# Kernel tuning notes

Hardware: AMD Instinct MI355X
Metric: run time of the kernel (lower is better)

Reference implementation:

```python
import jax, jax.numpy as jnp
import numpy as np
import math

B, C, H, W_ = 64, 1024, 10, 10      # C = vis_chans = ir_chans = lan_chans = m_chans
NTOK, MTOK = H * W_, 20             # 100 image tokens (W1: 100x100), 20 text tokens (W2: 100x20)
K_NN, BIG, EPS = 8, 1.0e6, 1e-8


def _minmax(t):
    # per-sample min-max normalization over the full distance slice
    mn = t.min(axis=(1, 2), keepdims=True)
    mx = t.max(axis=(1, 2), keepdims=True)
    return (t - mn) / (mx - mn + EPS)


def _geodesic(X):
    # Isomap-style geodesic distances: symmetric 8-NN Euclidean graph + Floyd-Warshall.
    P = X.shape[0]
    sq = jnp.sum(X * X, axis=-1)
    D = jnp.sqrt(jnp.maximum(sq[:, None] + sq[None, :] - 2.0 * (X @ X.T), 0.0))
    Dm = D + jnp.eye(P, dtype=X.dtype) * BIG          # exclude self from kNN
    negd, idx = jax.lax.top_k(-Dm, K_NN)              # 8 nearest neighbors per node
    A = jnp.full((P, P), BIG, X.dtype).at[jnp.arange(P)[:, None], idx].set(-negd)
    Wg = jnp.minimum(A, A.T)                          # undirected graph
    Wg = Wg.at[jnp.diag_indices(P)].set(0.0)

    def body(Dk, k):
        return jnp.minimum(Dk, Dk[:, k][:, None] + Dk[k, :][None, :]), None

    Wg, _ = jax.lax.scan(body, Wg, jnp.arange(P))
    return Wg


def _forward(ir, vis, lan, vis_w, vis_b, vis_g, vis_be, ir_w, ir_b, ir_g, ir_be,
             t_w, t_b, vout_w, vout_b, tout_w, tout_b, W1, b1, W2, b2, W4, W5,
             ml_w, ml_b, ml2_w, ml2_b, scalars):
    lam1, lam2, a1, be1, g1, a2, be2, g2, wg_aw, wg_ab, wg_bw, wg_bb = scalars
    sqc = jnp.sqrt(jnp.float32(C))
    vis_r = vis.reshape(B, C, -1).transpose(0, 2, 1)   # [B,100,C]
    ir_r = ir.reshape(B, C, -1).transpose(0, 2, 1)     # [B,100,C]
    lan_t = lan.transpose(0, 2, 1)                     # [B,20,C]

    geo = jax.vmap(_geodesic)

    # ---- compute_M_image (detached in original) ----
    joint_vi = jnp.concatenate([vis_r, ir_r], axis=1)                    # [B,200,C]
    d_vi = jax.lax.stop_gradient(geo(joint_vi))[:, :NTOK, NTOK:]         # [B,100,100]
    M_v2i_dist = _minmax(d_vi)
    sigma = jax.lax.stop_gradient(jnp.median(M_v2i_dist))
    M_v2i_fix = jnp.exp(-M_v2i_dist ** 2 / (2.0 * sigma ** 2))
    lam1s = jax.nn.sigmoid(lam1)
    M_v2i_learn = lam1s * M_v2i_fix + (1.0 - lam1s) * (W1 * M_v2i_fix + b1)

    def conv_in_relu(x, w3, b3, g3, be3, i):
        # 1x1 conv + InstanceNorm2d(affine) + ReLU, flattened to tokens
        y = jnp.einsum('bchw,mc->bmhw', x, w3[i]) + b3[i][None, :, None, None]
        mu = y.mean((2, 3), keepdims=True)
        var = y.var((2, 3), keepdims=True)
        y = (y - mu) / jnp.sqrt(var + 1e-5) * g3[i][None, :, None, None] + be3[i][None, :, None, None]
        return jax.nn.relu(y).reshape(B, C, -1).transpose(0, 2, 1)       # [B,100,C]

    Qv, Kv, Vv = [conv_in_relu(vis, vis_w, vis_b, vis_g, vis_be, i) for i in range(3)]
    Qi, Ki, Vi = [conv_in_relu(ir, ir_w, ir_b, ir_g, ir_be, i) for i in range(3)]
    Qt, Kt, Vt = [jax.nn.relu(lan_t @ t_w[i].T + t_b[i]) for i in range(3)]

    # fusion weights from GAP of the learned manifold matrix
    Mgap = M_v2i_learn.mean((1, 2), keepdims=True)       # [B,1,1]
    alpha = jax.nn.sigmoid(wg_aw * Mgap + wg_ab)
    beta = jax.nn.sigmoid(wg_bw * Mgap + wg_bb)
    Qf, Kf, Vf = alpha * Qv + beta * Qi, alpha * Kv + beta * Ki, alpha * Vv + beta * Vi
    feat_img = alpha * vis_r + beta * ir_r               # [B,100,C]

    # ---- compute_M_text (detached in original) ----
    joint_it = jnp.concatenate([feat_img, lan_t], axis=1)                # [B,120,C]
    d_it = jax.lax.stop_gradient(geo(joint_it))
    M_i2t_dist = _minmax(d_it[:, :NTOK, NTOK:])          # [B,100,20] (unused downstream, as in original)
    M_t2i_dist = _minmax(d_it[:, NTOK:, :NTOK])          # [B,20,100]
    sigma2 = jax.lax.stop_gradient(jnp.median(M_t2i_dist))
    M_t2i_fix = jnp.exp(-M_t2i_dist ** 2 / (2.0 * sigma2 ** 2))          # [B,20,100]
    M_i2t_fix = M_t2i_fix.transpose(0, 2, 1)                             # [B,100,20]
    lam2s = jax.nn.sigmoid(lam2)
    M_i2t_lo = lam2s * M_i2t_fix + (1.0 - lam2s) * (W2 * M_i2t_fix + b2) # [B,100,20]
    M_t2i_lo = M_i2t_lo.transpose(0, 2, 1)                               # [B,20,100]
    M_t2i_lo = jax.nn.softmax(M_t2i_lo / sqc, axis=2)
    M_i2t_lo = jax.nn.softmax(M_i2t_lo / sqc, axis=2)
    M_t2i_learn = (M_i2t_lo @ lan_t) @ ml_w.T + ml_b       # [B,100,C]
    M_i2t_learn = (M_t2i_lo @ feat_img) @ ml2_w.T + ml2_b  # [B,20,C]

    # ---- text->image cross attention ----
    A = Qt @ Kf.transpose(0, 2, 1) \
        + a1 * (Qt @ M_t2i_learn.transpose(0, 2, 1)) \
        + be1 * (W4 @ (M_t2i_learn @ Kf.transpose(0, 2, 1)))
    Av = jax.nn.softmax(A / sqc, axis=2)                   # [B,20,100]
    new_lan = Av @ Vf + g1 * (M_t2i_lo @ Vf)               # [B,20,C]

    # ---- image->text cross attention ----
    Bm = Qf @ Kt.transpose(0, 2, 1) \
        + a2 * (Qf @ M_i2t_learn.transpose(0, 2, 1)) \
        + be2 * (W5 @ (M_i2t_learn @ Kt.transpose(0, 2, 1)))
    Bv = jax.nn.softmax(Bm / sqc, axis=2)                  # [B,100,20]
    new_vis = Bv @ Vt + g2 * (M_i2t_lo @ Vt)               # [B,100,C]

    new_vis = new_vis.transpose(0, 2, 1).reshape(B, C, H, W_)
    new_vis = jnp.einsum('bchw,mc->bmhw', new_vis, vout_w) + vout_b[None, :, None, None]
    new_lan = new_lan @ tout_w.T + tout_b

    # ---- regularization loss ----
    fA = jax.nn.softmax(M_t2i_fix / sqc, axis=2)
    fB = jax.nn.softmax(M_i2t_fix / sqc, axis=2)
    l1 = jnp.abs(Av - fA).mean() + jnp.abs(Bv - fB).mean()
    var = lambda x: jnp.var(x, ddof=1)                    # torch .var() is unbiased
    l2 = -jnp.abs(var(Av) - var(fA)) - jnp.abs(var(Bv) - var(fB))
    loss = (l1 + 100.0 * l2) * 1000.0
    return new_vis, new_lan, loss


def setup_inputs() -> dict:
    key = jax.random.key(0)
    ks = jax.random.split(key, 20)
    f = lambda k, s, sc=1.0: jax.random.normal(k, s, jnp.float32) * sc
    return dict(
        ir=f(ks[0], (B, C, H, W_)),
        vis=f(ks[1], (B, C, H, W_)),
        lan=f(ks[2], (B, C, MTOK)),
        vis_w=f(ks[3], (3, C, C), 0.02), vis_b=jnp.zeros((3, C), jnp.float32),
        vis_g=jnp.ones((3, C), jnp.float32), vis_be=jnp.zeros((3, C), jnp.float32),
        ir_w=f(ks[4], (3, C, C), 0.02), ir_b=jnp.zeros((3, C), jnp.float32),
        ir_g=jnp.ones((3, C), jnp.float32), ir_be=jnp.zeros((3, C), jnp.float32),
        t_w=f(ks[5], (3, C, C), 0.02), t_b=jnp.zeros((3, C), jnp.float32),
        vout_w=f(ks[6], (C, C), 0.02), vout_b=jnp.zeros((C,), jnp.float32),
        tout_w=f(ks[7], (C, C), 0.02), tout_b=jnp.zeros((C,), jnp.float32),
        W1=f(ks[8], (NTOK, NTOK), 0.1), b1=jnp.zeros((NTOK, NTOK), jnp.float32),
        W2=f(ks[9], (NTOK, MTOK), 0.1), b2=jnp.zeros((NTOK, MTOK), jnp.float32),
        W4=f(ks[10], (MTOK, NTOK), 0.1),
        W5=f(ks[11], (NTOK, MTOK), 0.1),
        ml_w=f(ks[12], (C, C), 0.02), ml_b=jnp.zeros((C,), jnp.float32),
        ml2_w=f(ks[13], (C, C), 0.02), ml2_b=jnp.zeros((C,), jnp.float32),
        # [lam1, lam2, a1, b1, g1, a2, b2, g2, wg_aw, wg_ab, wg_bw, wg_bb]
        scalars=jnp.array([0.5, 0.5, 0.5, 0.5, 0.5, 0.5, 0.5, 0.5, 0.3, 0.0, 0.3, 0.0], jnp.float32),
    )


def reference(ir, vis, lan, vis_w, vis_b, vis_g, vis_be, ir_w, ir_b, ir_g, ir_be,
              t_w, t_b, vout_w, vout_b, tout_w, tout_b, W1, b1, W2, b2, W4, W5,
              ml_w, ml_b, ml2_w, ml2_b, scalars):
    return _forward(ir, vis, lan, vis_w, vis_b, vis_g, vis_be, ir_w, ir_b, ir_g, ir_be,
                    t_w, t_b, vout_w, vout_b, tout_w, tout_b, W1, b1, W2, b2, W4, W5,
                    ml_w, ml_b, ml2_w, ml2_b, scalars)
```

## Files before the change

### kernel.cpp

```cpp
#include <hip/hip_runtime.h>
#include <hip/hip_bf16.h>
#include <math.h>

#define B_   64
#define C_   1024
#define HW   100
#define MT_  20
#define P1   200
#define P2   120
#define BIGF 1.0e6f
#define EPSF 1e-8f
#define SQC  32.0f

static constexpr size_t F_J    = 0;
static constexpr size_t N_J    = (size_t)B_*P1*C_;
static constexpr size_t F_D    = F_J + N_J;
static constexpr size_t N_D    = (size_t)B_*P1*P1;
static constexpr size_t F_SQ   = F_D + N_D;
static constexpr size_t N_SQ   = (size_t)B_*P1;
static constexpr size_t F_KNN  = F_SQ + N_SQ;
static constexpr size_t N_KNN  = (size_t)B_*P1*8;
static constexpr size_t F_MV   = F_KNN + N_KNN;
static constexpr size_t N_MV   = (size_t)B_*HW*HW;
static constexpr size_t F_MT   = F_MV + N_MV;
// ... 71 lines not shown
  int row = blockIdx.x;
  const float* r = J + (size_t)row*C_;
  float s = 0.f;
  for (int c = threadIdx.x; c < C_; c += 64){ float v = r[c]; s += v*v; }
  for (int o = 32; o > 0; o >>= 1) s += __shfl_down(s, o);
  if (threadIdx.x == 0) sq[row] = s;
}

__global__ __launch_bounds__(256) void k_gram_dist(const float* __restrict__ J,
    const float* __restrict__ sq, float* __restrict__ D, int P){
  __shared__ __align__(16) float Xi[32][68];
  __shared__ __align__(16) float Xj[32][68];
  int b = blockIdx.z;
  int r0 = blockIdx.x*64, s0 = blockIdx.y*64;
  int tx = threadIdx.x & 15, ty = threadIdx.x >> 4;
  const float* Jb = J + (size_t)b*P*C_;
  float acc[4][4];
  #pragma unroll
  for (int u = 0; u < 4; u++)
    #pragma unroll
    for (int v = 0; v < 4; v++) acc[u][v] = 0.f;
  for (int c0 = 0; c0 < C_; c0 += 32){
    for (int e = threadIdx.x; e < 2048; e += 256){
      int rr = e >> 5, cc = e & 31;
      Xi[cc][rr] = (r0+rr < P) ? Jb[(size_t)(r0+rr)*C_ + c0+cc] : 0.f;
      Xj[cc][rr] = (s0+rr < P) ? Jb[(size_t)(s0+rr)*C_ + c0+cc] : 0.f;
    }
    __syncthreads();
    for (int kk = 0; kk < 32; kk++){
      float4 xr4 = *(const float4*)&Xi[kk][ty*4];
      float4 xs4 = *(const float4*)&Xj[kk][tx*4];
      float xr[4] = {xr4.x, xr4.y, xr4.z, xr4.w};
      float xs[4] = {xs4.x, xs4.y, xs4.z, xs4.w};
      #pragma unroll
      for (int u = 0; u < 4; u++)
        #pragma unroll
        for (int v = 0; v < 4; v++) acc[u][v] += xr[u]*xs[v];
    }
    __syncthreads();
  }
  #pragma unroll
  for (int u = 0; u < 4; u++){
    #pragma unroll
    for (int v = 0; v < 4; v++){
      int r = r0 + ty*4 + u, s = s0 + tx*4 + v;
      if (r < P && s < P){
        float d2 = sq[b*P+r] + sq[b*P+s] - 2.f*acc[u][v];
        D[((size_t)b*P + r)*P + s] = sqrtf(fmaxf(d2, 0.f));
      }
    }
  }
}

template<int P>
__global__ void k_knn(const float* __restrict__ D, int* __restrict__ knn){
  constexpr int NS = (P + 63)/64;
  int row = blockIdx.x;
  int i = row % P;
  const float* Dr = D + (size_t)row*P;
  float v[NS];
  #pragma unroll
  for (int t = 0; t < NS; t++){
    int j = threadIdx.x + t*64;
    float d = (j < P) ? Dr[j] : 4.0e6f;
    if (j == i) d += BIGF;
    v[t] = d;
  }
  for (int k = 0; k < 8; k++){
    float bv = 3.4e38f; int bj = 1 << 30;
    #pragma unroll
    for (int t = 0; t < NS; t++){
      int j = threadIdx.x + t*64;
      if (v[t] < bv){ bv = v[t]; bj = j; }
    }
    for (int o = 32; o > 0; o >>= 1){
      float ov = __shfl_xor(bv, o);
      int   oj = __shfl_xor(bj, o);
      if (ov < bv || (ov == bv && oj < bj)){ bv = ov; bj = oj; }
    }
    if (threadIdx.x == 0) knn[(size_t)row*8 + k] = bj;
    if ((bj & 63) == (int)threadIdx.x){
      #pragma unroll
      for (int t = 0; t < NS; t++) if (t == (bj >> 6)) v[t] = 3.9e38f;
    }
  }
}

template<int P, int NT, int RP, int CP, int R0, int C0, int RR, int CC>
__global__ __launch_bounds__(1024) void k_fwx(const float* __restrict__ D,
    const int* __restrict__ knn, float* __restrict__ outM){
  constexpr int PR = P/RP;
  constexpr int PC = P/CP;
  constexpr int NTH = PR*PC;
  __shared__ float rowk[P], colk[P];
  __shared__ int kl[P*8];
  __shared__ float rmn[1024], rmx[1024];
  int b = blockIdx.x;
  const float* Db = D + (size_t)b*P*P;
  const int* kb = knn + (size_t)b*P*8;
  int tid = threadIdx.x;
  bool act = tid < NTH;
  int pi = tid / PC, pj = tid - pi*PC;
  int i0 = pi*RP, j0 = pj*CP;
  for (int e = tid; e < P*8; e += NT) kl[e] = kb[e];
  __syncthreads();
  float w[RP][CP];
  if (act){
    #pragma unroll
    for (int r = 0; r < RP; r++){
      float4 v = *(const float4*)(Db + (size_t)(i0+r)*P + j0);
      w[r][0]=v.x; w[r][1]=v.y; w[r][2]=v.z; w[r][3]=v.w;
      int i = i0 + r;
      #pragma unroll
      for (int c = 0; c < CP; c++){
        int j = j0 + c;
        if (i == j) w[r][c] = 0.f;
        else {
          const int* ki = &kl[i*8];
          const int* kj = &kl[j*8];
          bool e = false;
          #pragma unroll
          for (int k = 0; k < 8; k++) e = e || (ki[k] == j) || (kj[k] == i);
          if (!e) w[r][c] = BIGF;
        }
      }
    }
  }
  __syncthreads();
  for (int k = 0; k < P; k++){
    if (act){
      #pragma unroll
      for (int r = 0; r < RP; r++){
        if (i0 + r == k)
          *(float4*)(rowk + j0) = make_float4(w[r][0],w[r][1],w[r][2],w[r][3]);
      }
      #pragma unroll
      for (int c = 0; c < CP; c++){
        if (j0 + c == k){
          #pragma unroll
          for (int r = 0; r < RP; r++) colk[i0+r] = w[r][c];
        }
      }
    }
    __syncthreads();
    if (act){
      float4 rk4 = *(const float4*)(rowk + j0);
      float rk[4] = {rk4.x, rk4.y, rk4.z, rk4.w};
      float ck[RP];
      #pragma unroll
      for (int r = 0; r < RP; r++) ck[r] = colk[i0+r];
      #pragma unroll
      for (int r = 0; r < RP; r++)
        #pragma unroll
        for (int c = 0; c < CP; c++)
          w[r][c] = fminf(w[r][c], ck[r] + rk[c]);
    }
    __syncthreads();
  }
  float mn = 3.4e38f, mx = -3.4e38f;
  if (act){
    #pragma unroll
    for (int r = 0; r < RP; r++){
      int i = i0 + r;
      if (i >= R0 && i < R0+RR){
        #pragma unroll
        for (int c = 0; c < CP; c++){
          int j = j0 + c;
          if (j >= C0 && j < C0+CC){
            mn = fminf(mn, w[r][c]); mx = fmaxf(mx, w[r][c]);
          }
        }
      }
    }
  }
  rmn[tid] = mn; rmx[tid] = mx;
  __syncthreads();
  for (int o = 512; o > 0; o >>= 1){
    if (tid < o && tid + o < NT){
      rmn[tid] = fminf(rmn[tid], rmn[tid+o]);
      rmx[tid] = fmaxf(rmx[tid], rmx[tid+o]);
    }
    __syncthreads();
  }
  mn = rmn[0]; mx = rmx[0];
  float inv = 1.f/(mx - mn + EPSF);
  if (act){
    #pragma unroll
    for (int r = 0; r < RP; r++){
      int i = i0 + r;
      if (i >= R0 && i < R0+RR){
        #pragma unroll
        for (int c = 0; c < CP; c++){
          int j = j0 + c;
          if (j >= C0 && j < C0+CC)
            outM[((size_t)b*RR + (i-R0))*CC + (j-C0)] = (w[r][c] - mn)*inv;
        }
      }
    }
  }
}

__global__ void k_med_init(float* hs){ if (threadIdx.x == 0){ hs[0] = 0.f; hs[1] = 1.0f; } }

__global__ __launch_bounds__(256) void k_med_hist(const float* __restrict__ x, int N,
                           const float* __restrict__ hs, unsigned* __restrict__ hist){
  __shared__ unsigned lh[1025];
  for (int i = threadIdx.x; i < 1025; i += 256) lh[i] = 0u;
  __syncthreads();
  float lo = hs[0], hi = hs[1];
  float scale = 1024.f/(hi - lo);
  unsigned below = 0;
  int idx = blockIdx.x*256 + threadIdx.x;
  int stride = gridDim.x*256;
  for (int i = idx; i < N; i += stride){
    float v = x[i];
    if (v < lo) below++;
    else if (v < hi){
      int bn = (int)((v - lo)*scale);
      if (bn > 1023) bn = 1023;
      atomicAdd(&lh[bn], 1u);
    }
  }
  for (int o = 32; o > 0; o >>= 1) below += __shfl_down(below, o);
  if ((threadIdx.x & 63) == 0 && below) atomicAdd(&lh[1024], below);
  __syncthreads();
  for (int i = threadIdx.x; i < 1025; i += 256){
    unsigned v = lh[i];
    if (v) atomicAdd(&hist[i], v);
  }
}

__global__ void k_med_select(float* hs, const unsigned* __restrict__ hist, int k){
  if (threadIdx.x != 0) return;
  float lo = hs[0], hi = hs[1], w = (hi - lo)*(1.f/1024.f);
  unsigned cum = hist[1024];
  int bf = 1023;
  for (int bn = 0; bn < 1024; bn++){
    unsigned h = hist[bn];
    if (cum + h > (unsigned)k){ bf = bn; break; }
    cum += h;
  }
  hs[0] = lo + bf*w; hs[1] = lo + (bf+1)*w;
}

__global__ __launch_bounds__(256) void k_mgap(const float* __restrict__ Mv,
    const float* __restrict__ W1, const float* __restrict__ b1,
    const float* __restrict__ sc, const float* __restrict__ hs,
    float* __restrict__ alpha, float* __restrict__ bet){
  __shared__ float sr[256];
  int b = blockIdx.x;
  float lam1s = 1.f/(1.f + expf(-sc[0]));
  float sig = 0.5f*(hs[0] + hs[1]);
  float inv2s = 1.f/(2.f*sig*sig);
  const float* Mb = Mv + (size_t)b*HW*HW;
  float s = 0.f;
  for (int e = threadIdx.x; e < HW*HW; e += 256){
    float v = Mb[e];
    float f = expf(-v*v*inv2s);
    s += lam1s*f + (1.f - lam1s)*(W1[e]*f + b1[e]);
  }
  sr[threadIdx.x] = s; __syncthreads();
  for (int o = 128; o > 0; o >>= 1){
    if ((int)threadIdx.x < o) sr[threadIdx.x] += sr[threadIdx.x+o];
    __syncthreads();
  }
  if (threadIdx.x == 0){
    float mg = sr[0]*(1.f/(HW*HW));
    alpha[b] = 1.f/(1.f + expf(-(sc[8]*mg + sc[9])));
    bet[b]   = 1.f/(1.f + expf(-(sc[10]*mg + sc[11])));
  }
}

__global__ void k_castw(const float* __restrict__ a, const float* __restrict__ b,
                        short* __restrict__ oa, short* __restrict__ ob){
  int i = (blockIdx.x*256 + threadIdx.x)*4;
  if (i >= 3*C_*C_) return;
  float4 va = *(const float4*)(a + i);
  float4 vb = *(const float4*)(b + i);
  short ra[4] = { f2bf(va.x), f2bf(va.y), f2bf(va.z), f2bf(va.w) };
  short rb[4] = { f2bf(vb.x), f2bf(vb.y), f2bf(vb.z), f2bf(vb.w) };
  *(bhalf*)(oa + i) = *(bhalf*)ra;
  *(bhalf*)(ob + i) = *(bhalf*)rb;
}

__global__ void k_cast(const float* __restrict__ a, short* __restrict__ oa, int n){
  int i = (blockIdx.x*256 + threadIdx.x)*4;
  if (i >= n) return;
  float4 va = *(const float4*)(a + i);
  short ra[4] = { f2bf(va.x), f2bf(va.y), f2bf(va.z), f2bf(va.w) };
  *(bhalf*)(oa + i) = *(bhalf*)ra;
}

__global__ void k_cast2(const float* __restrict__ a, const float* __restrict__ b,
                        short* __restrict__ oa, short* __restrict__ ob,
                        int n1, int n2){
// ... 91 lines not shown
      bfrag axv = zf, axi = zf;
      if (tf*16 + lr < HW){
        axv = *(const bfrag*)(xvp + (size_t)tf*16*C_ + k0);
        axi = *(const bfrag*)(xip + (size_t)tf*16*C_ + k0);
      }
      acc[tf][0][0] = MFMA_B16(axv, bw0v, acc[tf][0][0]);
      acc[tf][1][0] = MFMA_B16(axv, bw1v, acc[tf][1][0]);
      acc[tf][0][1] = MFMA_B16(axi, bw0i, acc[tf][0][1]);
      acc[tf][1][1] = MFMA_B16(axi, bw1i, acc[tf][1][1]);
    }
  }
  float al = alpha[b], bt = bet[b];
  float* ob = out + ((size_t)(wsel*B_ + b))*HW*C_;
  #pragma unroll
  for (int mf = 0; mf < 2; mf++){
    int m = m0 + w*32 + mf*16 + lr;
    float s1v=0.f,s2v=0.f,s1i=0.f,s2i=0.f;
    #pragma unroll
    for (int tf = 0; tf < 7; tf++){
      #pragma unroll
      for (int r = 0; r < 4; r++){
        int t = tf*16 + lg*4 + r;
        if (t < HW){
          float yv = acc[tf][mf][0][r], yi = acc[tf][mf][1][r];
          s1v += yv; s2v += yv*yv; s1i += yi; s2i += yi*yi;
        }
      }
    }
    s1v += __shfl_xor(s1v,16); s1v += __shfl_xor(s1v,32);
    s2v += __shfl_xor(s2v,16); s2v += __shfl_xor(s2v,32);
    s1i += __shfl_xor(s1i,16); s1i += __shfl_xor(s1i,32);
    s2i += __shfl_xor(s2i,16); s2i += __shfl_xor(s2i,32);
    float muv = s1v*0.01f, varv = s2v*0.01f - muv*muv;
    float mui = s1i*0.01f, vari = s2i*0.01f - mui*mui;
    float scv = vg[wsel*C_+m]/sqrtf(varv+1e-5f);
    float shv = vbe[wsel*C_+m] - muv*scv;
    float sci = ig[wsel*C_+m]/sqrtf(vari+1e-5f);
    float shi = ibe[wsel*C_+m] - mui*sci;
    #pragma unroll
    for (int tf = 0; tf < 7; tf++){
      #pragma unroll
      for (int r = 0; r < 4; r++){
        int t = tf*16 + lg*4 + r;
        if (t < HW){
          float yv = fmaxf(acc[tf][mf][0][r]*scv + shv, 0.f);
          float yi = fmaxf(acc[tf][mf][1][r]*sci + shi, 0.f);
          ob[(size_t)t*C_ + m] = al*yv + bt*yi;
        }
      }
    }
  }
}

__global__ __launch_bounds__(256) void k_s3_mfma(
    const float* __restrict__ Ml, const float* __restrict__ Kf,
    float* __restrict__ S3){
  int jt = blockIdx.x, b = blockIdx.y;
  int tid = threadIdx.x;
  int lane = tid & 63, w = tid >> 6;
  int lg = lane >> 4, lr = lane & 15;
  f32x4 acc[7];
  #pragma unroll
  for (int tf = 0; tf < 7; tf++) acc[tf] = (f32x4){0.f,0.f,0.f,0.f};
  const float* Ab = Ml + (size_t)b*HW*C_;
  const float* Bb = Kf + (size_t)b*HW*C_;
  const bfrag zf = {0,0,0,0,0,0,0,0};
  int j = jt*64 + w*16 + lr;
  for (int k0 = 0; k0 < C_; k0 += 32){
    int kc = k0 + lg*8;
    bfrag bw = zf;
    if (j < HW){
      float4 u = *(const float4*)(Bb + (size_t)j*C_ + kc);
      float4 v = *(const float4*)(Bb + (size_t)j*C_ + kc + 4);
      bw[0]=f2bf(u.x); bw[1]=f2bf(u.y); bw[2]=f2bf(u.z); bw[3]=f2bf(u.w);
      bw[4]=f2bf(v.x); bw[5]=f2bf(v.y); bw[6]=f2bf(v.z); bw[7]=f2bf(v.w);
    }
    #pragma unroll
    for (int tf = 0; tf < 7; tf++){
      bfrag fa = zf;
      int i = tf*16 + lr;
      if (i < HW){
        float4 u = *(const float4*)(Ab + (size_t)i*C_ + kc);
        float4 v = *(const float4*)(Ab + (size_t)i*C_ + kc + 4);
        fa[0]=f2bf(u.x); fa[1]=f2bf(u.y); fa[2]=f2bf(u.z); fa[3]=f2bf(u.w);
        fa[4]=f2bf(v.x); fa[5]=f2bf(v.y); fa[6]=f2bf(v.z); fa[7]=f2bf(v.w);
      }
      acc[tf] = MFMA_B16(fa, bw, acc[tf]);
    }
  }
  float* ob = S3 + (size_t)b*HW*HW;
  #pragma unroll
  for (int tf = 0; tf < 7; tf++){
    #pragma unroll
    for (int r = 0; r < 4; r++){
      int i = tf*16 + lg*4 + r;
      if (i < HW && j < HW) ob[(size_t)i*HW + j] = acc[tf][r];
    }
  }
}

__global__ __launch_bounds__(256) void k_tokproj_mfma(
    const float* __restrict__ X, const short* __restrict__ W16,
    const float* __restrict__ bias, float* __restrict__ out){
  constexpr int NROW = B_*MT_;
  int n0 = blockIdx.x*128;
  int t0 = blockIdx.y*112;
  int tid = threadIdx.x;
  int lane = tid & 63, w = tid >> 6;
  int lg = lane >> 4, lr = lane & 15;
  f32x4 acc[7][2];
  #pragma unroll
  for (int tf = 0; tf < 7; tf++)
    #pragma unroll
    for (int mf = 0; mf < 2; mf++)
      acc[tf][mf] = (f32x4){0.f,0.f,0.f,0.f};
  const short* wp = W16 + (size_t)(n0 + w*32 + lr)*C_ + lg*8;
  const bfrag zf = {0,0,0,0,0,0,0,0};
  for (int k0 = 0; k0 < C_; k0 += 32){
    bfrag bw0 = *(const bfrag*)(wp + k0);
    bfrag bw1 = *(const bfrag*)(wp + (size_t)16*C_ + k0);
    #pragma unroll
    for (int tf = 0; tf < 7; tf++){
      bfrag ax = zf;
      int row = t0 + tf*16 + lr;
      if (row < NROW){
        const float* ap = X + (size_t)row*C_ + k0 + lg*8;
        float4 u = *(const float4*)ap;
        float4 v = *(const float4*)(ap + 4);
        ax[0]=f2bf(u.x); ax[1]=f2bf(u.y); ax[2]=f2bf(u.z); ax[3]=f2bf(u.w);
        ax[4]=f2bf(v.x); ax[5]=f2bf(v.y); ax[6]=f2bf(v.z); ax[7]=f2bf(v.w);
      }
      acc[tf][0] = MFMA_B16(ax, bw0, acc[tf][0]);
      acc[tf][1] = MFMA_B16(ax, bw1, acc[tf][1]);
    }
  }
  #pragma unroll
  for (int mf = 0; mf < 2; mf++){
    int n = n0 + w*32 + mf*16 + lr;
    float bv = bias[n];
    #pragma unroll
    for (int tf = 0; tf < 7; tf++){
      #pragma unroll
      for (int r = 0; r < 4; r++){
        int row = t0 + tf*16 + lg*4 + r;
        if (row < NROW) out[(size_t)row*C_ + n] = acc[tf][mf][r] + bv;
      }
    }
  }
}

#define TPAD 36
__global__ __launch_bounds__(256) void k_convout_mfma(
    const short* __restrict__ NVb, const short* __restrict__ Wb,
// ... 121 lines not shown
  }
}

__global__ void k_mfixppre(const float* __restrict__ Mt, const float* __restrict__ hs2,
                           const float* __restrict__ W2, const float* __restrict__ b2,
                           const float* __restrict__ sc,
                           float* __restrict__ Mfix, float* __restrict__ Ppre){
  int idx = blockIdx.x*256 + threadIdx.x;
  if (idx >= B_*MT_*HW) return;
  int i = idx % HW;
  int j = (idx/HW) % MT_;
  int b = idx/(MT_*HW);
  float sig = 0.5f*(hs2[0] + hs2[1]);
  float v = Mt[idx];
  float f = expf(-v*v/(2.f*sig*sig));
  Mfix[idx] = f;
  float lam2s = 1.f/(1.f + expf(-sc[1]));
  Ppre[((size_t)b*HW + i)*MT_ + j] = lam2s*f + (1.f - lam2s)*(W2[i*MT_ + j]*f + b2[i*MT_ + j]);
}

__global__ __launch_bounds__(256) void k_sm20(const float* __restrict__ Ppre, float* __restrict__ Pi2t){
  int row = blockIdx.x*8 + (threadIdx.x >> 5);
  int lane = threadIdx.x & 31;
  if (row >= B_*HW) return;
  float v = (lane < MT_) ? Ppre[(size_t)row*MT_ + lane]*(1.f/SQC) : -3.4e38f;
  float m = v;
  for (int o = 16; o > 0; o >>= 1) m = fmaxf(m, __shfl_xor(m, o, 32));
  float e = (lane < MT_) ? expf(v - m) : 0.f;
  float s = e;
  for (int o = 16; o > 0; o >>= 1) s += __shfl_xor(s, o, 32);
  if (lane < MT_) Pi2t[(size_t)row*MT_ + lane] = e/s;
}

__global__ __launch_bounds__(128) void k_smT(const float* __restrict__ Ppre, float* __restrict__ Pt2i){
  __shared__ float sm[128], ss[128];
  int bj = blockIdx.x; int b = bj/MT_, j = bj % MT_;
  int i = threadIdx.x;
  float v = (i < HW) ? Ppre[((size_t)b*HW + i)*MT_ + j]*(1.f/SQC) : -3.4e38f;
  sm[i] = v; __syncthreads();
  for (int o = 64; o > 0; o >>= 1){
    if (i < o) sm[i] = fmaxf(sm[i], sm[i+o]);
    __syncthreads();
  }
  float m = sm[0];
  float e = (i < HW) ? expf(v - m) : 0.f;
  ss[i] = e; __syncthreads();
  for (int o = 64; o > 0; o >>= 1){
    if (i < o) ss[i] += ss[i+o];
    __syncthreads();
  }
  if (i < HW) Pt2i[((size_t)b*MT_ + j)*HW + i] = e/ss[0];
}

__global__ __launch_bounds__(256) void k_mlearn_t2i(const float* __restrict__ Pi2t,
    const float* __restrict__ lanML, const float* __restrict__ mlb, float* __restrict__ out){
  __shared__ float sP[HW][MT_];
  int b = blockIdx.y; int m = blockIdx.x*256 + threadIdx.x;
  for (int e = threadIdx.x; e < HW*MT_; e += 256) sP[e/MT_][e%MT_] = Pi2t[(size_t)b*HW*MT_ + e];
  __syncthreads();
  float vL[MT_];
  #pragma unroll
  for (int j = 0; j < MT_; j++) vL[j] = lanML[((size_t)b*MT_ + j)*C_ + m];
  float bb = mlb[m];
  for (int i = 0; i < HW; i++){
    float a = bb;
    #pragma unroll
    for (int j = 0; j < MT_; j++) a += sP[i][j]*vL[j];
    out[((size_t)b*HW + i)*C_ + m] = a;
  }
}

__global__ __launch_bounds__(256) void k_t2(const float* __restrict__ Pt2i,
    const float* __restrict__ feat, float* __restrict__ T2o){
  __shared__ float sP[MT_][HW];
  int b = blockIdx.y; int m = blockIdx.x*256 + threadIdx.x;
  for (int e = threadIdx.x; e < MT_*HW; e += 256) sP[e/HW][e%HW] = Pt2i[(size_t)b*MT_*HW + e];
  __syncthreads();
  float acc[MT_];
  #pragma unroll
  for (int j = 0; j < MT_; j++) acc[j] = 0.f;
  for (int i = 0; i < HW; i++){
    float f = feat[((size_t)b*HW + i)*C_ + m];
    #pragma unroll
    for (int j = 0; j < MT_; j++) acc[j] += sP[j][i]*f;
  }
  #pragma unroll
  for (int j = 0; j < MT_; j++) T2o[((size_t)b*MT_ + j)*C_ + m] = acc[j];
}

__global__ __launch_bounds__(256) void k_abt(const float* __restrict__ X,
    const float* __restrict__ Y, float* __restrict__ out, int I, int Jd){
  __shared__ float Xs[16][33], Ys[64][33];
  int i0 = blockIdx.x*16, j0 = blockIdx.y*64, b = blockIdx.z;
  int jl = threadIdx.x & 63, ig = threadIdx.x >> 6;
  float acc[4] = {0.f,0.f,0.f,0.f};
  const float* Xb = X + (size_t)b*I*C_;
  const float* Yb = Y + (size_t)b*Jd*C_;
  for (int c0 = 0; c0 < C_; c0 += 32){
    for (int e = threadIdx.x; e < 512; e += 256){
      int r = e >> 5, cc = e & 31;
      Xs[r][cc] = (i0+r < I) ? Xb[(size_t)(i0+r)*C_ + c0+cc] : 0.f;
    }
    for (int e = threadIdx.x; e < 2048; e += 256){
      int r = e >> 5, cc = e & 31;
      Ys[r][cc] = (j0+r < Jd) ? Yb[(size_t)(j0+r)*C_ + c0+cc] : 0.f;
    }
    __syncthreads();
    for (int kk = 0; kk < 32; kk++){
      float y = Ys[jl][kk];
      #pragma unroll
      for (int k = 0; k < 4; k++) acc[k] += Xs[ig*4+k][kk]*y;
    }
    __syncthreads();
  }
  #pragma unroll
  for (int k = 0; k < 4; k++){
    int i = i0 + ig*4 + k, j = j0 + jl;
    if (i < I && j < Jd) out[((size_t)b*I + i)*Jd + j] = acc[k];
  }
}

__global__ __launch_bounds__(256) void k_abt2(const float* __restrict__ X,
    const float* __restrict__ Y1, const float* __restrict__ Y2,
    float* __restrict__ out1, float* __restrict__ out2, int I, int Jd){
  __shared__ float Xs[16][33], Y1s[64][33], Y2s[64][33];
  int i0 = blockIdx.x*16, j0 = blockIdx.y*64, b = blockIdx.z;
  int jl = threadIdx.x & 63, ig = threadIdx.x >> 6;
  float acc1[4] = {0.f,0.f,0.f,0.f};
  float acc2[4] = {0.f,0.f,0.f,0.f};
  const float* Xb  = X  + (size_t)b*I*C_;
  const float* Y1b = Y1 + (size_t)b*Jd*C_;
  const float* Y2b = Y2 + (size_t)b*Jd*C_;
  for (int c0 = 0; c0 < C_; c0 += 32){
    for (int e = threadIdx.x; e < 512; e += 256){
      int r = e >> 5, cc = e & 31;
      Xs[r][cc] = (i0+r < I) ? Xb[(size_t)(i0+r)*C_ + c0+cc] : 0.f;
    }
    for (int e = threadIdx.x; e < 2048; e += 256){
      int r = e >> 5, cc = e & 31;
      bool ok = (j0+r < Jd);
      Y1s[r][cc] = ok ? Y1b[(size_t)(j0+r)*C_ + c0+cc] : 0.f;
      Y2s[r][cc] = ok ? Y2b[(size_t)(j0+r)*C_ + c0+cc] : 0.f;
    }
    __syncthreads();
    for (int kk = 0; kk < 32; kk++){
      float y1 = Y1s[jl][kk], y2 = Y2s[jl][kk];
      #pragma unroll
      for (int k = 0; k < 4; k++){
        float x = Xs[ig*4+k][kk];
        acc1[k] += x*y1;
        acc2[k] += x*y2;
      }
    }
    __syncthreads();
  }
  #pragma unroll
  for (int k = 0; k < 4; k++){
    int i = i0 + ig*4 + k, j = j0 + jl;
    if (i < I && j < Jd){
      out1[((size_t)b*I + i)*Jd + j] = acc1[k];
      out2[((size_t)b*I + i)*Jd + j] = acc2[k];
    }
  }
}

__global__ __launch_bounds__(128) void k_attA(const float* __restrict__ S1,
    const float* __restrict__ S2, const float* __restrict__ S3,
    const float* __restrict__ W4, const float* __restrict__ sc,
    const float* __restrict__ Mfix, float* __restrict__ Av, float* __restrict__ pa){
  __shared__ float red[128];
  int bq = blockIdx.x; int b = bq/MT_, q = bq % MT_;
  int j = threadIdx.x;
  float a1 = sc[2], be1 = sc[3];
  float v = -3.4e38f;
  if (j < HW){
    float s3 = 0.f;
    const float* S3b = S3 + (size_t)b*HW*HW + j;
    const float* w4 = W4 + (size_t)q*HW;
    for (int p = 0; p < HW; p++) s3 += w4[p]*S3b[(size_t)p*HW];
    size_t off = ((size_t)b*MT_ + q)*HW + j;
    v = (S1[off] + a1*S2[off] + be1*s3)*(1.f/SQC);
  }
  red[j] = v; __syncthreads();
  for (int o = 64; o > 0; o >>= 1){
    if (j < o) red[j] = fmaxf(red[j], red[j+o]);
    __syncthreads();
  }
  float m = red[0]; __syncthreads();
  float e = (j < HW) ? expf(v - m) : 0.f;
  red[j] = e; __syncthreads();
  for (int o = 64; o > 0; o >>= 1){
    if (j < o) red[j] += red[j+o];
    __syncthreads();
  }
  float av = (j < HW) ? e/red[0] : 0.f;
  if (j < HW) Av[((size_t)b*MT_ + q)*HW + j] = av;
  __syncthreads();
  float vm = (j < HW) ? Mfix[(size_t)bq*HW + j]*(1.f/SQC) : -3.4e38f;
  red[j] = vm; __syncthreads();
  for (int o = 64; o > 0; o >>= 1){
    if (j < o) red[j] = fmaxf(red[j], red[j+o]);
    __syncthreads();
  }
  float mm = red[0]; __syncthreads();
  float em = (j < HW) ? expf(vm - mm) : 0.f;
  red[j] = em; __syncthreads();
  for (int o = 64; o > 0; o >>= 1){
    if (j < o) red[j] += red[j+o];
    __syncthreads();
  }
  float fa = (j < HW) ? em/red[0] : 0.f;
  __syncthreads();
  float p[5] = { fabsf(av - fa), av, av*av, fa, fa*fa };
  for (int s = 0; s < 5; s++){
    red[j] = p[s]; __syncthreads();
    for (int o = 64; o > 0; o >>= 1){
      if (j < o) red[j] += red[j+o];
      __syncthreads();
    }
    if (j == 0) pa[bq*5 + s] = red[0];
    __syncthreads();
  }
}

__global__ __launch_bounds__(256) void k_attB(const float* __restrict__ S4a,
    const float* __restrict__ S4b, const float* __restrict__ S5,
    const float* __restrict__ W5, const float* __restrict__ sc,
    const float* __restrict__ Mfix, float* __restrict__ Bv, float* __restrict__ pb){
  __shared__ float red[8];
  int row = blockIdx.x*8 + (threadIdx.x >> 5);
  int lane = threadIdx.x & 31;
  int b = row/HW, i = row % HW;
  float a2 = sc[5], be2 = sc[6];
  float v = -3.4e38f;
  if (lane < MT_){
    float s5 = 0.f;
    const float* S5b = S5 + (size_t)b*MT_*MT_ + lane;
    const float* w5 = W5 + (size_t)i*MT_;
    #pragma unroll
    for (int p = 0; p < MT_; p++) s5 += w5[p]*S5b[p*MT_];
    size_t off = (size_t)row*MT_ + lane;
    v = (S4a[off] + a2*S4b[off] + be2*s5)*(1.f/SQC);
  }
  float m = v;
  for (int o = 16; o > 0; o >>= 1) m = fmaxf(m, __shfl_xor(m, o, 32));
  float e = (lane < MT_) ? expf(v - m) : 0.f;
  float s = e;
  for (int o = 16; o > 0; o >>= 1) s += __shfl_xor(s, o, 32);
  float bv = (lane < MT_) ? e/s : 0.f;
// ... 82 lines not shown
    red[threadIdx.x] = t[k]; __syncthreads();
    for (int o = 128; o > 0; o >>= 1){
      if ((int)threadIdx.x < o) red[threadIdx.x] += red[threadIdx.x+o];
      __syncthreads();
    }
    res[5+k] = red[0]; __syncthreads();
  }
  if (threadIdx.x == 0){
    const float n = 128000.f;
    float l1 = res[0]/n + res[5]/n;
    float varAv = (res[2] - res[1]*res[1]/n)/(n - 1.f);
    float varfA = (res[4] - res[3]*res[3]/n)/(n - 1.f);
    float varBv = (res[7] - res[6]*res[6]/n)/(n - 1.f);
    float varfB = (res[9] - res[8]*res[8]/n)/(n - 1.f);
    float l2 = -fabsf(varAv - varfA) - fabsf(varBv - varfB);
    outloss[0] = (l1 + 100.f*l2)*1000.f;
  }
}

extern "C" void kernel_launch(void* const* d_in, const int* in_sizes, int n_in,
                              void* d_out, int out_size, void* d_ws, size_t ws_size,
                              hipStream_t stream){
  const float* ir     = (const float*)d_in[0];
  const float* vis    = (const float*)d_in[1];
  const float* lan    = (const float*)d_in[2];
  const float* vis_w  = (const float*)d_in[3];
  const float* vis_g  = (const float*)d_in[5];
  const float* vis_be = (const float*)d_in[6];
  const float* ir_w   = (const float*)d_in[7];
  const float* ir_g   = (const float*)d_in[9];
  const float* ir_be  = (const float*)d_in[10];
  const float* t_w    = (const float*)d_in[11];
  const float* t_b    = (const float*)d_in[12];
  const float* vout_w = (const float*)d_in[13];
  const float* vout_b = (const float*)d_in[14];
  const float* tout_w = (const float*)d_in[15];
  const float* tout_b = (const float*)d_in[16];
  const float* W1     = (const float*)d_in[17];
  const float* b1     = (const float*)d_in[18];
  const float* W2     = (const float*)d_in[19];
  const float* b2     = (const float*)d_in[20];
  const float* W4     = (const float*)d_in[21];
  const float* W5     = (const float*)d_in[22];
  const float* ml_w   = (const float*)d_in[23];
  const float* ml_b   = (const float*)d_in[24];
  const float* ml2_w  = (const float*)d_in[25];
  const float* ml2_b  = (const float*)d_in[26];
  const float* sc     = (const float*)d_in[27];

  float* ws = (float*)d_ws;
  float* J     = ws + F_J;
  float* Dm    = ws + F_D;
  float* sqb   = ws + F_SQ;
  int*   knn   = (int*)(ws + F_KNN);
  float* Mv    = ws + F_MV;
  float* Mt    = ws + F_MT;
  float* Mfix  = ws + F_MFIX;
  float* QKVf  = ws + F_QKVF;
  float* QKVt  = ws + F_QKVT;
  float* feat  = ws + F_FEAT;
  float* lanML = ws + F_LANML;
  float* T2b   = ws + F_T2;
  float* Mi2tL = ws + F_MI2TL;
  float* S1    = ws + F_S1;
  float* S2    = ws + F_S2;
  float* S4a   = ws + F_S4A;
  float* S4b   = ws + F_S4B;
  float* S5    = ws + F_S5;
  float* Av    = ws + F_AV;
  float* Bv    = ws + F_BV;
  float* NL    = ws + F_NL;
  float* alpha = ws + F_AL;
  float* bet   = ws + F_BE;
  float* hs    = ws + F_HS;
  unsigned* hist = (unsigned*)(ws + F_HIST);
  float* pa    = ws + F_PA;
  float* pb    = ws + F_PB;
  float* MlT2I = ws + F_J;
  float* S3    = ws + F_D;
  float* Pi2t  = ws + F_MV;
  float* Pt2i  = ws + F_MV + 128000;
  float* Ppre  = ws + F_MV + 256000;
  short* XtV    = (short*)(ws + F_J);
  short* XtI    = (short*)(ws + F_J + 3300000);
  short* WVb    = (short*)(ws + F_J + 6600000);
  short* WIb    = (short*)(ws + F_J + 8200000);
  short* NVb    = (short*)(ws + F_J + 6553600);
  short* Wob16  = (short*)(ws + F_J + 9830400);
  short* lanTb  = (short*)(ws + F_J + 10360000);
  short* Wtb    = (short*)(ws + F_D);
  short* tout16 = (short*)(ws + F_D + 1000000);
  short* ml2w16 = (short*)(ws + F_D + 1530000);

  float* out_vis  = (float*)d_out;
  float* out_lan  = out_vis + (size_t)B_*C_*HW;
  float* out_loss = out_lan + (size_t)B_*MT_*C_;

  float* Qf = QKVf;
  float* Kf = QKVf + (size_t)B_*HW*C_;
  float* Vf = QKVf + (size_t)2*B_*HW*C_;
  float* Qt = QKVt;
  float* Kt = QKVt + (size_t)B_*MT_*C_;
  float* Vt = QKVt + (size_t)2*B_*MT_*C_;

  k_pack_j1<<<dim3(32,7,B_),256,0,stream>>>(vis, ir, J);
  k_rowsq<<<B_*P1,64,0,stream>>>(J, sqb, P1);
  k_gram_dist<<<dim3(4,4,B_),256,0,stream>>>(J, sqb, Dm, P1);
  k_knn<P1><<<B_*P1,64,0,stream>>>(Dm, knn);
  k_fwx<P1,1024,10,4,0,100,100,100><<<B_,1024,0,stream>>>(Dm, knn, Mv);
  k_med_init<<<1,64,0,stream>>>(hs);
  for (int it = 0; it < 2; it++){
    hipMemsetAsync(hist, 0, 1025*sizeof(unsigned), stream);
    k_med_hist<<<256,256,0,stream>>>(Mv, B_*HW*HW, hs, hist);
    k_med_select<<<1,64,0,stream>>>(hs, hist, B_*HW*HW/2);
  }
  k_mgap<<<B_,256,0,stream>>>(Mv, W1, b1, sc, hs, alpha, bet);

  k_castw<<<(3*C_*C_/4+255)/256,256,0,stream>>>(vis_w, ir_w, WVb, WIb);
  k_cast<<<(C_*C_/4+255)/256,256,0,stream>>>(vout_w, Wob16, C_*C_);
  k_cast2<<<((4*C_*C_)/4+255)/256,256,0,stream>>>(t_w, ml_w, Wtb,
                                                  Wtb + (size_t)3*C_*C_,
                                                  3*C_*C_, C_*C_);
  k_xt2<<<dim3(32,4,B_),256,0,stream>>>(vis, ir, alpha, bet, XtV, XtI, feat);
  k_lanT<<<dim3(32,B_),256,0,stream>>>(lan, lanTb);
  k_convqkv_mfma<<<dim3(8,3,B_),256,0,stream>>>(XtV, XtI, WVb, WIb,
                                                vis_g, vis_be, ir_g, ir_be,
                                                alpha, bet, QKVf);
  k_textproj_mfma<<<dim3(8,12,4),256,0,stream>>>(lanTb, Wtb, t_b, QKVt, lanML);
  k_cast2<<<((2*C_*C_)/4+255)/256,256,0,stream>>>(tout_w, ml2_w, tout16, ml2w16,
                                                  C_*C_, C_*C_);

  k_pack_j2<<<(B_*P2*C_+255)/256,256,0,stream>>>(feat, lan, J);
  k_rowsq<<<B_*P2,64,0,stream>>>(J, sqb, P2);
  k_gram_dist<<<dim3(2,2,B_),256,0,stream>>>(J, sqb, Dm, P2);
  k_knn<P2><<<B_*P2,64,0,stream>>>(Dm, knn);
  k_fwx<P2,960,4,4,100,0,MT_,100><<<B_,960,0,stream>>>(Dm, knn, Mt);
  k_med_init<<<1,64,0,stream>>>(hs+2);
  for (int it = 0; it < 2; it++){
    hipMemsetAsync(hist, 0, 1025*sizeof(unsigned), stream);
    k_med_hist<<<256,256,0,stream>>>(Mt, B_*MT_*HW, hs+2, hist);
    k_med_select<<<1,64,0,stream>>>(hs+2, hist, B_*MT_*HW/2);
  }
  k_mfixppre<<<(B_*MT_*HW+255)/256,256,0,stream>>>(Mt, hs+2, W2, b2, sc, Mfix, Ppre);
  k_sm20<<<(B_*HW+7)/8,256,0,stream>>>(Ppre, Pi2t);
  k_smT<<<B_*MT_,128,0,stream>>>(Ppre, Pt2i);

  k_mlearn_t2i<<<dim3(4,B_),256,0,stream>>>(Pi2t, lanML, ml_b, MlT2I);
  k_t2<<<dim3(4,B_),256,0,stream>>>(Pt2i, feat, T2b);
  k_tokproj_mfma<<<dim3(8,12),256,0,stream>>>(T2b, ml2w16, ml2_b, Mi2tL);

  k_abt2<<<dim3(2,2,B_),256,0,stream>>>(Qt, Kf, MlT2I, S1, S2, MT_, HW);
  k_s3_mfma<<<dim3(2,B_),256,0,stream>>>(MlT2I, Kf, S3);
  k_abt2<<<dim3(7,1,B_),256,0,stream>>>(Qf, Kt, Mi2tL, S4a, S4b, HW, MT_);
  k_abt<<<dim3(2,1,B_),256,0,stream>>>(Mi2tL, Kt, S5, MT_, MT_);
  k_attA<<<B_*MT_,128,0,stream>>>(S1, S2, S3, W4, sc, Mfix, Av, pa);
  k_attB<<<B_*HW/8,256,0,stream>>>(S4a, S4b, S5, W5, sc, Mfix, Bv, pb);

  k_nl<<<dim3(4,B_),256,0,stream>>>(Av, Pt2i, Vf, sc, NL);
  k_nv<<<dim3(4,B_),256,0,stream>>>(Bv, Pi2t, Vt, sc, NVb);
  k_tokproj_mfma<<<dim3(8,12),256,0,stream>>>(NL, tout16, tout_b, out_lan);
  k_convout_mfma<<<dim3(8,B_),256,0,stream>>>(NVb, Wob16, vout_b, out_vis);

  k_loss_final<<<1,256,0,stream>>>(pa, pb, out_loss);
}
```

Before: 2.606 ms.

## Fuse kNN into Floyd-Warshall, reassociate S3 product, merge small kernels

```diff
diff --git a/kernel.cpp b/kernel.cpp
--- a/kernel.cpp
+++ b/kernel.cpp
@@ -147,43 +147,9 @@
   }
 }
 
-template<int P>
-__global__ void k_knn(const float* __restrict__ D, int* __restrict__ knn){
-  constexpr int NS = (P + 63)/64;
-  int row = blockIdx.x;
-  int i = row % P;
-  const float* Dr = D + (size_t)row*P;
-  float v[NS];
-  #pragma unroll
-  for (int t = 0; t < NS; t++){
-    int j = threadIdx.x + t*64;
-    float d = (j < P) ? Dr[j] : 4.0e6f;
-    if (j == i) d += BIGF;
-    v[t] = d;
-  }
-  for (int k = 0; k < 8; k++){
-    float bv = 3.4e38f; int bj = 1 << 30;
-    #pragma unroll
-    for (int t = 0; t < NS; t++){
-      int j = threadIdx.x + t*64;
-      if (v[t] < bv){ bv = v[t]; bj = j; }
-    }
-    for (int o = 32; o > 0; o >>= 1){
-      float ov = __shfl_xor(bv, o);
-      int   oj = __shfl_xor(bj, o);
-      if (ov < bv || (ov == bv && oj < bj)){ bv = ov; bj = oj; }
-    }
-    if (threadIdx.x == 0) knn[(size_t)row*8 + k] = bj;
-    if ((bj & 63) == (int)threadIdx.x){
-      #pragma unroll
-      for (int t = 0; t < NS; t++) if (t == (bj >> 6)) v[t] = 3.9e38f;
-    }
-  }
-}
-
 template<int P, int NT, int RP, int CP, int R0, int C0, int RR, int CC>
 __global__ __launch_bounds__(1024) void k_fwx(const float* __restrict__ D,
-    const int* __restrict__ knn, float* __restrict__ outM){
+    float* __restrict__ outM, float* __restrict__ hs, unsigned* __restrict__ hist){
   constexpr int PR = P/RP;
   constexpr int PC = P/CP;
   constexpr int NTH = PR*PC;
@@ -192,13 +158,32 @@
   __shared__ float rmn[1024], rmx[1024];
   int b = blockIdx.x;
   const float* Db = D + (size_t)b*P*P;
-  const int* kb = knn + (size_t)b*P*8;
   int tid = threadIdx.x;
+  if (b == 0){
+    for (int e = tid; e < 1025; e += NT) hist[e] = 0u;
+    if (tid == 0){ hs[0] = 0.f; hs[1] = 1.0f; }
+  }
+  if (tid < P){
+    int chosen[8];
+    const float* Dr = Db + (size_t)tid*P;
+    for (int k = 0; k < 8; k++){
+      float bv = 3.4e38f; int bj = 1 << 30;
+      for (int j = 0; j < P; j++){
+        float d = Dr[j];
+        if (j == tid) d += BIGF;
+        bool sk = false;
+        #pragma unroll
+        for (int c = 0; c < 8; c++) if (c < k) sk = sk || (chosen[c] == j);
+        if (!sk && d < bv){ bv = d; bj = j; }
+      }
+      chosen[k] = bj;
+      kl[tid*8 + k] = bj;
+    }
+  }
+  __syncthreads();
   bool act = tid < NTH;
   int pi = tid / PC, pj = tid - pi*PC;
   int i0 = pi*RP, j0 = pj*CP;
-  for (int e = tid; e < P*8; e += NT) kl[e] = kb[e];
-  __syncthreads();
   float w[RP][CP];
   if (act){
     #pragma unroll
@@ -294,8 +279,6 @@
     }
   }
 }
-
-__global__ void k_med_init(float* hs){ if (threadIdx.x == 0){ hs[0] = 0.f; hs[1] = 1.0f; } }
 
 __global__ __launch_bounds__(256) void k_med_hist(const float* __restrict__ x, int N,
                            const float* __restrict__ hs, unsigned* __restrict__ hist){
@@ -325,17 +308,20 @@
   }
 }
 
-__global__ void k_med_select(float* hs, const unsigned* __restrict__ hist, int k){
-  if (threadIdx.x != 0) return;
-  float lo = hs[0], hi = hs[1], w = (hi - lo)*(1.f/1024.f);
-  unsigned cum = hist[1024];
-  int bf = 1023;
-  for (int bn = 0; bn < 1024; bn++){
-    unsigned h = hist[bn];
-    if (cum + h > (unsigned)k){ bf = bn; break; }
-    cum += h;
-  }
-  hs[0] = lo + bf*w; hs[1] = lo + (bf+1)*w;
+__global__ void k_med_select(float* hs, unsigned* __restrict__ hist, int k){
+  if (threadIdx.x == 0){
+    float lo = hs[0], hi = hs[1], w = (hi - lo)*(1.f/1024.f);
+    unsigned cum = hist[1024];
+    int bf = 1023;
+    for (int bn = 0; bn < 1024; bn++){
+      unsigned h = hist[bn];
+      if (cum + h > (unsigned)k){ bf = bn; break; }
+      cum += h;
+    }
+    hs[0] = lo + bf*w; hs[1] = lo + (bf+1)*w;
+  }
+  __syncthreads();
+  for (int i = threadIdx.x; i < 1025; i += 64) hist[i] = 0u;
 }
 
 __global__ __launch_bounds__(256) void k_mgap(const float* __restrict__ Mv,
@@ -533,53 +519,6 @@
   }
 }
 
-__global__ __launch_bounds__(256) void k_s3_mfma(
-    const float* __restrict__ Ml, const float* __restrict__ Kf,
-    float* __restrict__ S3){
-  int jt = blockIdx.x, b = blockIdx.y;
-  int tid = threadIdx.x;
-  int lane = tid & 63, w = tid >> 6;
-  int lg = lane >> 4, lr = lane & 15;
-  f32x4 acc[7];
-  #pragma unroll
-  for (int tf = 0; tf < 7; tf++) acc[tf] = (f32x4){0.f,0.f,0.f,0.f};
-  const float* Ab = Ml + (size_t)b*HW*C_;
-  const float* Bb = Kf + (size_t)b*HW*C_;
-  const bfrag zf = {0,0,0,0,0,0,0,0};
-  int j = jt*64 + w*16 + lr;
-  for (int k0 = 0; k0 < C_; k0 += 32){
-    int kc = k0 + lg*8;
-    bfrag bw = zf;
-    if (j < HW){
-      float4 u = *(const float4*)(Bb + (size_t)j*C_ + kc);
-      float4 v = *(const float4*)(Bb + (size_t)j*C_ + kc + 4);
-      bw[0]=f2bf(u.x); bw[1]=f2bf(u.y); bw[2]=f2bf(u.z); bw[3]=f2bf(u.w);
-      bw[4]=f2bf(v.x); bw[5]=f2bf(v.y); bw[6]=f2bf(v.z); bw[7]=f2bf(v.w);
-    }
-    #pragma unroll
-    for (int tf = 0; tf < 7; tf++){
-      bfrag fa = zf;
-      int i = tf*16 + lr;
-      if (i < HW){
-        float4 u = *(const float4*)(Ab + (size_t)i*C_ + kc);
-        float4 v = *(const float4*)(Ab + (size_t)i*C_ + kc + 4);
-        fa[0]=f2bf(u.x); fa[1]=f2bf(u.y); fa[2]=f2bf(u.z); fa[3]=f2bf(u.w);
-        fa[4]=f2bf(v.x); fa[5]=f2bf(v.y); fa[6]=f2bf(v.z); fa[7]=f2bf(v.w);
-      }
-      acc[tf] = MFMA_B16(fa, bw, acc[tf]);
-    }
-  }
-  float* ob = S3 + (size_t)b*HW*HW;
-  #pragma unroll
-  for (int tf = 0; tf < 7; tf++){
-    #pragma unroll
-    for (int r = 0; r < 4; r++){
-      int i = tf*16 + lg*4 + r;
-      if (i < HW && j < HW) ob[(size_t)i*HW + j] = acc[tf][r];
-    }
-  }
-}
-
 __global__ __launch_bounds__(256) void k_tokproj_mfma(
     const float* __restrict__ X, const short* __restrict__ W16,
     const float* __restrict__ bias, float* __restrict__ out){
@@ -807,40 +746,55 @@
   if (i < HW) Pt2i[((size_t)b*MT_ + j)*HW + i] = e/ss[0];
 }
 
-__global__ __launch_bounds__(256) void k_mlearn_t2i(const float* __restrict__ Pi2t,
-    const float* __restrict__ lanML, const float* __restrict__ mlb, float* __restrict__ out){
+__global__ __launch_bounds__(256) void k_mlearn2(const float* __restrict__ Pi2t,
+    const float* __restrict__ Pt2i, const float* __restrict__ lanML,
+    const float* __restrict__ mlb, const float* __restrict__ feat,
+    float* __restrict__ outMl, float* __restrict__ T2o){
   __shared__ float sP[HW][MT_];
+  __shared__ float sQ[MT_][HW];
   int b = blockIdx.y; int m = blockIdx.x*256 + threadIdx.x;
-  for (int e = threadIdx.x; e < HW*MT_; e += 256) sP[e/MT_][e%MT_] = Pi2t[(size_t)b*HW*MT_ + e];
+  for (int e = threadIdx.x; e < HW*MT_; e += 256){
+    sP[e/MT_][e%MT_] = Pi2t[(size_t)b*HW*MT_ + e];
+    sQ[e/HW][e%HW]   = Pt2i[(size_t)b*MT_*HW + e];
+  }
   __syncthreads();
   float vL[MT_];
   #pragma unroll
   for (int j = 0; j < MT_; j++) vL[j] = lanML[((size_t)b*MT_ + j)*C_ + m];
+  float accT[MT_];
+  #pragma unroll
+  for (int j = 0; j < MT_; j++) accT[j] = 0.f;
   float bb = mlb[m];
   for (int i = 0; i < HW; i++){
+    float f = feat[((size_t)b*HW + i)*C_ + m];
     float a = bb;
     #pragma unroll
-    for (int j = 0; j < MT_; j++) a += sP[i][j]*vL[j];
-    out[((size_t)b*HW + i)*C_ + m] = a;
-  }
-}
-
-__global__ __launch_bounds__(256) void k_t2(const float* __restrict__ Pt2i,
-    const float* __restrict__ feat, float* __restrict__ T2o){
-  __shared__ float sP[MT_][HW];
+    for (int j = 0; j < MT_; j++){
+      a += sP[i][j]*vL[j];
+      accT[j] += sQ[j][i]*f;
+    }
+    outMl[((size_t)b*HW + i)*C_ + m] = a;
+  }
+  #pragma unroll
+  for (int j = 0; j < MT_; j++) T2o[((size_t)b*MT_ + j)*C_ + m] = accT[j];
+}
+
+__global__ __launch_bounds__(256) void k_w4ml(const float* __restrict__ W4,
+    const float* __restrict__ Ml, float* __restrict__ out){
+  __shared__ float sW[MT_][HW];
   int b = blockIdx.y; int m = blockIdx.x*256 + threadIdx.x;
-  for (int e = threadIdx.x; e < MT_*HW; e += 256) sP[e/HW][e%HW] = Pt2i[(size_t)b*MT_*HW + e];
+  for (int e = threadIdx.x; e < MT_*HW; e += 256) sW[e/HW][e%HW] = W4[e];
   __syncthreads();
   float acc[MT_];
   #pragma unroll
   for (int j = 0; j < MT_; j++) acc[j] = 0.f;
-  for (int i = 0; i < HW; i++){
-    float f = feat[((size_t)b*HW + i)*C_ + m];
-    #pragma unroll
-    for (int j = 0; j < MT_; j++) acc[j] += sP[j][i]*f;
-  }
-  #pragma unroll
-  for (int j = 0; j < MT_; j++) T2o[((size_t)b*MT_ + j)*C_ + m] = acc[j];
+  for (int p = 0; p < HW; p++){
+    float f = Ml[((size_t)b*HW + p)*C_ + m];
+    #pragma unroll
+    for (int j = 0; j < MT_; j++) acc[j] += sW[j][p]*f;
+  }
+  #pragma unroll
+  for (int j = 0; j < MT_; j++) out[((size_t)b*MT_ + j)*C_ + m] = acc[j];
 }
 
 __global__ __launch_bounds__(256) void k_abt(const float* __restrict__ X,
@@ -920,21 +874,17 @@
 }
 
 __global__ __launch_bounds__(128) void k_attA(const float* __restrict__ S1,
-    const float* __restrict__ S2, const float* __restrict__ S3,
-    const float* __restrict__ W4, const float* __restrict__ sc,
-    const float* __restrict__ Mfix, float* __restrict__ Av, float* __restrict__ pa){
+    const float* __restrict__ S2, const float* __restrict__ S3n,
+    const float* __restrict__ sc, const float* __restrict__ Mfix,
+    float* __restrict__ Av, float* __restrict__ pa){
   __shared__ float red[128];
-  int bq = blockIdx.x; int b = bq/MT_, q = bq % MT_;
+  int bq = blockIdx.x;
   int j = threadIdx.x;
   float a1 = sc[2], be1 = sc[3];
   float v = -3.4e38f;
   if (j < HW){
-    float s3 = 0.f;
-    const float* S3b = S3 + (size_t)b*HW*HW + j;
-    const float* w4 = W4 + (size_t)q*HW;
-    for (int p = 0; p < HW; p++) s3 += w4[p]*S3b[(size_t)p*HW];
-    size_t off = ((size_t)b*MT_ + q)*HW + j;
-    v = (S1[off] + a1*S2[off] + be1*s3)*(1.f/SQC);
+    size_t off = (size_t)bq*HW + j;
+    v = (S1[off] + a1*S2[off] + be1*S3n[off])*(1.f/SQC);
   }
   red[j] = v; __syncthreads();
   for (int o = 64; o > 0; o >>= 1){
@@ -949,7 +899,7 @@
     __syncthreads();
   }
   float av = (j < HW) ? e/red[0] : 0.f;
-  if (j < HW) Av[((size_t)b*MT_ + q)*HW + j] = av;
+  if (j < HW) Av[(size_t)bq*HW + j] = av;
   __syncthreads();
   float vm = (j < HW) ? Mfix[(size_t)bq*HW + j]*(1.f/SQC) : -3.4e38f;
   red[j] = vm; __syncthreads();
@@ -1138,7 +1088,6 @@
   float* J     = ws + F_J;
   float* Dm    = ws + F_D;
   float* sqb   = ws + F_SQ;
-  int*   knn   = (int*)(ws + F_KNN);
   float* Mv    = ws + F_MV;
   float* Mt    = ws + F_MT;
   float* Mfix  = ws + F_MFIX;
@@ -1163,7 +1112,8 @@
   float* pa    = ws + F_PA;
   float* pb    = ws + F_PB;
   float* MlT2I = ws + F_J;
-  float* S3    = ws + F_D;
+  float* S3n   = ws + F_D;
+  float* W4Ml  = ws + F_T2;
   float* Pi2t  = ws + F_MV;
   float* Pt2i  = ws + F_MV + 128000;
   float* Ppre  = ws + F_MV + 256000;
@@ -1192,11 +1142,8 @@
   k_pack_j1<<<dim3(32,7,B_),256,0,stream>>>(vis, ir, J);
   k_rowsq<<<B_*P1,64,0,stream>>>(J, sqb, P1);
   k_gram_dist<<<dim3(4,4,B_),256,0,stream>>>(J, sqb, Dm, P1);
-  k_knn<P1><<<B_*P1,64,0,stream>>>(Dm, knn);
-  k_fwx<P1,1024,10,4,0,100,100,100><<<B_,1024,0,stream>>>(Dm, knn, Mv);
-  k_med_init<<<1,64,0,stream>>>(hs);
+  k_fwx<P1,1024,10,4,0,100,100,100><<<B_,1024,0,stream>>>(Dm, Mv, hs, hist);
   for (int it = 0; it < 2; it++){
-    hipMemsetAsync(hist, 0, 1025*sizeof(unsigned), stream);
     k_med_hist<<<256,256,0,stream>>>(Mv, B_*HW*HW, hs, hist);
     k_med_select<<<1,64,0,stream>>>(hs, hist, B_*HW*HW/2);
   }
@@ -1219,11 +1166,8 @@
   k_pack_j2<<<(B_*P2*C_+255)/256,256,0,stream>>>(feat, lan, J);
   k_rowsq<<<B_*P2,64,0,stream>>>(J, sqb, P2);
   k_gram_dist<<<dim3(2,2,B_),256,0,stream>>>(J, sqb, Dm, P2);
-  k_knn<P2><<<B_*P2,64,0,stream>>>(Dm, knn);
-  k_fwx<P2,960,4,4,100,0,MT_,100><<<B_,960,0,stream>>>(Dm, knn, Mt);
-  k_med_init<<<1,64,0,stream>>>(hs+2);
+  k_fwx<P2,960,4,4,100,0,MT_,100><<<B_,960,0,stream>>>(Dm, Mt, hs+2, hist);
   for (int it = 0; it < 2; it++){
-    hipMemsetAsync(hist, 0, 1025*sizeof(unsigned), stream);
     k_med_hist<<<256,256,0,stream>>>(Mt, B_*MT_*HW, hs+2, hist);
     k_med_select<<<1,64,0,stream>>>(hs+2, hist, B_*MT_*HW/2);
   }
@@ -1231,15 +1175,15 @@
   k_sm20<<<(B_*HW+7)/8,256,0,stream>>>(Ppre, Pi2t);
   k_smT<<<B_*MT_,128,0,stream>>>(Ppre, Pt2i);
 
-  k_mlearn_t2i<<<dim3(4,B_),256,0,stream>>>(Pi2t, lanML, ml_b, MlT2I);
-  k_t2<<<dim3(4,B_),256,0,stream>>>(Pt2i, feat, T2b);
+  k_mlearn2<<<dim3(4,B_),256,0,stream>>>(Pi2t, Pt2i, lanML, ml_b, feat, MlT2I, T2b);
   k_tokproj_mfma<<<dim3(8,12),256,0,stream>>>(T2b, ml2w16, ml2_b, Mi2tL);
 
+  k_w4ml<<<dim3(4,B_),256,0,stream>>>(W4, MlT2I, W4Ml);
   k_abt2<<<dim3(2,2,B_),256,0,stream>>>(Qt, Kf, MlT2I, S1, S2, MT_, HW);
-  k_s3_mfma<<<dim3(2,B_),256,0,stream>>>(MlT2I, Kf, S3);
+  k_abt<<<dim3(2,2,B_),256,0,stream>>>(W4Ml, Kf, S3n, MT_, HW);
   k_abt2<<<dim3(7,1,B_),256,0,stream>>>(Qf, Kt, Mi2tL, S4a, S4b, HW, MT_);
   k_abt<<<dim3(2,1,B_),256,0,stream>>>(Mi2tL, Kt, S5, MT_, MT_);
-  k_attA<<<B_*MT_,128,0,stream>>>(S1, S2, S3, W4, sc, Mfix, Av, pa);
+  k_attA<<<B_*MT_,128,0,stream>>>(S1, S2, S3n, sc, Mfix, Av, pa);
   k_attB<<<B_*HW/8,256,0,stream>>>(S4a, S4b, S5, W5, sc, Mfix, Bv, pb);
 
   k_nl<<<dim3(4,B_),256,0,stream>>>(Av, Pt2i, Vf, sc, NL);
```

After: 2.742 ms. +5.2%, slower.
